# Kernel tuning notes

Measured on AMD Instinct MI355X. Metric: run time of the kernel, lower is better.

## Reference

```python
import jax, jax.numpy as jnp
import numpy as np

B, Q, G, D = 32, 512, 100, 1024
SEED_COST_WEIGHT = 1.0
INF = jnp.float32(1e9)
PAD_COST = jnp.float32(1e3)  # constant cost on padded-GT rows; constant-per-row => does not perturb the valid assignment


def _hungarian(cost):
    """Optimal linear assignment via Jonker-Volgenant shortest augmenting path.
    cost: (n, m) float32 with n <= m. Every row gets a distinct column.
    Returns (m,) int32: 0-based row assigned to each column, -1 if column unassigned.
    Matches scipy.optimize.linear_sum_assignment on the transposed problem."""
    n, m = cost.shape
    cpad = jnp.pad(cost, ((1, 0), (0, 0)))            # 1-based row indexing
    u0 = jnp.zeros(n + 1, cost.dtype)                 # row potentials
    v0 = jnp.zeros(m + 1, cost.dtype)                 # col potentials
    p0 = jnp.zeros(m + 1, jnp.int32)                  # p[j]: 1-based row matched to col j (0 = free)

    def assign_row(i, uvp):
        u, v, p = uvp
        p = p.at[0].set(i)
        state = (u, v, p,
                 jnp.full(m + 1, INF, cost.dtype),    # minv: min reduced cost to reach col j
                 jnp.zeros(m + 1, bool),              # used cols
                 jnp.zeros(m + 1, jnp.int32),         # way: predecessor col on shortest path
                 jnp.int32(0))                        # j0: current col (0 = virtual start)

        def not_free(c):
            _, _, p, _, _, _, j0 = c
            return c[2][j0] != 0

        def step(c):
            u, v, p, minv, used, way, j0 = c
            used = used.at[j0].set(True)
            i0 = p[j0]
            cur = cpad[i0] - u[i0] - v[1:]            # reduced costs of row i0, shape (m,)
            upd = (~used[1:]) & (cur < minv[1:])
            minv = minv.at[1:].set(jnp.where(upd, cur, minv[1:]))
            way = way.at[1:].set(jnp.where(upd, j0, way[1:]))
            masked = jnp.where(used[1:], INF, minv[1:])
            j1 = jnp.argmin(masked).astype(jnp.int32) + 1
            delta = masked[j1 - 1]
            u = u.at[p].add(jnp.where(used, delta, jnp.float32(0.0)))
            v = jnp.where(used, v - delta, v)
            minv = jnp.where(used, minv, minv - delta)
            return (u, v, p, minv, used, way, j1)

        u, v, p, _, _, way, j0 = jax.lax.while_loop(not_free, step, state)

        def backtrack(c):
            j0, p = c
            j1 = way[j0]
            return (j1, p.at[j0].set(p[j1]))

        _, p = jax.lax.while_loop(lambda c: c[0] != 0, backtrack, (j0, p))
        return (u, v, p)

    _, _, p = jax.lax.fori_loop(1, n + 1, assign_row, (u0, v0, p0))
    return p[1:] - 1                                   # (m,) 0-based row per column, -1 if none


def _match(q_sig_flat, gt_sigs_norm, gt_pad_mask, q_seed_logits_flat):
    # Cost built transposed as (B, G, Q): rows = GT slots (n = G <= m = Q).
    # pairwise_similarity(metric='dot'): sim[q, g] = q_sig[q] . gt_sig[g]
    sim = jnp.einsum('bqd,bgd->bgq', q_sig_flat, gt_sigs_norm)   # (B, G, Q)
    cost = 1.0 - sim
    # seed cost is per-query: added to every GT row of that query's column
    cost = cost + SEED_COST_WEIGHT * (1.0 - jax.nn.sigmoid(q_seed_logits_flat))[:, None, :]
    # padded GT rows get a row-constant cost -> assignment over valid rows is unchanged
    cost = jnp.where(gt_pad_mask[:, :, None], cost, PAD_COST)
    row4col = jax.vmap(_hungarian)(jax.lax.stop_gradient(cost))  # (B, Q): GT idx per query
    safe = jnp.maximum(row4col, 0)
    valid = (row4col >= 0) & jnp.take_along_axis(gt_pad_mask, safe, axis=1)
    matched_query_mask = valid                                   # (B, Q) bool
    matched_gt_indices = jnp.where(valid, row4col, -1)           # (B, Q) int32, -1 = unmatched
    return matched_query_mask, matched_gt_indices


def setup_inputs() -> dict:
    key = jax.random.key(0)
    k1, k2, k3, k4 = jax.random.split(key, 4)
    q_sig_flat = jax.random.normal(k1, (B, Q, D), jnp.float32)
    gt = jax.random.normal(k2, (B, G, D), jnp.float32)
    gt_sigs_norm = gt / jnp.linalg.norm(gt, axis=-1, keepdims=True)  # 'norm' suffix -> unit vectors
    gt_pad_mask = jax.random.randint(k3, (B, G), 0, 2).astype(bool)  # True = valid GT
    q_seed_logits_flat = jax.random.normal(k4, (B, Q), jnp.float32)
    return {"q_sig_flat": q_sig_flat, "gt_sigs_norm": gt_sigs_norm,
            "gt_pad_mask": gt_pad_mask, "q_seed_logits_flat": q_seed_logits_flat}


def reference(q_sig_flat, gt_sigs_norm, gt_pad_mask, q_seed_logits_flat):
    return _match(q_sig_flat, gt_sigs_norm, gt_pad_mask, q_seed_logits_flat)
```

## Files before the change

### kernel.cpp

```cpp
#include <hip/hip_runtime.h>
#include <math.h>

#define B_ 32
#define Q_ 512
#define G_ 100
#define D_ 1024
#define INF_ 1.0e9f
#define NVCAP 96

typedef __attribute__((ext_vector_type(8))) short bf16x8;
typedef __attribute__((ext_vector_type(4))) float f32x4;

__device__ __forceinline__ void cvt_hilo(const float* a, bf16x8& hi, bf16x8& lo) {
#pragma unroll
    for (int j = 0; j < 8; ++j) {
        float x = a[j];
        unsigned u  = __float_as_uint(x);
        unsigned hb = (u + 0x7FFFu + ((u >> 16) & 1u)) >> 16;
        float hf = __uint_as_float(hb << 16);
        float r  = x - hf;
        unsigned v  = __float_as_uint(r);
        unsigned lb = (v + 0x7FFFu + ((v >> 16) & 1u)) >> 16;
        hi[j] = (short)hb;
        lo[j] = (short)lb;
    }
}

__global__ __launch_bounds__(512) void cost_kernel(
    const float* __restrict__ qsig, const float* __restrict__ gtm,
    const int* __restrict__ mask, const float* __restrict__ seed,
    float* __restrict__ cost)
{
    __shared__ float pool[27648];
    __shared__ int   vrow_s[128];
    __shared__ int   nv_s;

    const int b   = blockIdx.x;
    const int qt  = blockIdx.y;
    const int tid = threadIdx.x;

    if (tid < 64) {
        int base = 0;
#pragma unroll
        for (int hh = 0; hh < 2; ++hh) {
            int g = hh * 64 + tid;
            int m = (g < G_) ? mask[b * G_ + g] : 0;
            unsigned long long bal = __ballot(m != 0);
            int pre = base + __popcll(bal & ((1ull << tid) - 1ull));
            if (g < G_ && m != 0) vrow_s[pre] = g;
            base += __popcll(bal);
        }
        if (tid == 0) nv_s = (base < NVCAP) ? base : NVCAP;
    }
    __syncthreads();
    const int nv = nv_s;
    if (nv == 0) return;

    const int wid  = tid >> 6;
    const int lane = tid & 63;
    const int h    = wid & 1;
    const int sl   = wid >> 1;
    const int l15  = lane & 15;
    const int l4   = lane >> 4;

    float* qw  = pool + wid * 2304;
    float* gw  = pool + 18432 + wid * 1152;
    float* red = pool;

    const float* qbase = qsig + (size_t)(b * Q_ + qt * 64) * D_;
    const float* gbase = gtm  + (size_t)b * G_ * D_;

#pragma unroll 1
    for (int gtl = 0; gtl * 64 < nv; ++gtl) {
        const int sbase = gtl * 64;

        int grows_st[4];
#pragma unroll
        for (int it = 0; it < 4; ++it) {
            int slv = sbase + h * 32 + it * 8 + (lane >> 3);
            grows_st[it] = vrow_s[(slv < nv) ? slv : (nv - 1)];
        }

        f32x4 acc[2][4];
#pragma unroll
        for (int gi = 0; gi < 2; ++gi)
#pragma unroll
            for (int qj = 0; qj < 4; ++qj) acc[gi][qj] = (f32x4)0.0f;

#pragma unroll 1
        for (int t = 0; t < 8; ++t) {
            const int kt = sl * 256 + t * 32;
#pragma unroll
            for (int it = 0; it < 8; ++it) {
                int row = it * 8 + (lane >> 3);
                float4 v = *(const float4*)(qbase + (size_t)row * D_ + kt + 4 * (lane & 7));
                *(float4*)(qw + row * 36 + 4 * (lane & 7)) = v;
            }
#pragma unroll
            for (int it = 0; it < 4; ++it) {
                int row = it * 8 + (lane >> 3);
                float4 v = *(const float4*)(gbase + (size_t)grows_st[it] * D_ + kt + 4 * (lane & 7));
                *(float4*)(gw + row * 36 + 4 * (lane & 7)) = v;
            }
            bf16x8 bh[4], bl[4];
#pragma unroll
            for (int qj = 0; qj < 4; ++qj) {
                float tmp[8];
                const float* qr = qw + (qj * 16 + l15) * 36 + l4 * 8;
                *(float4*)&tmp[0] = *(const float4*)qr;
                *(float4*)&tmp[4] = *(const float4*)(qr + 4);
                cvt_hilo(tmp, bh[qj], bl[qj]);
            }
#pragma unroll
            for (int gi = 0; gi < 2; ++gi) {
                float tmp[8];
                const float* gr = gw + (gi * 16 + l15) * 36 + l4 * 8;
                *(float4*)&tmp[0] = *(const float4*)gr;
                *(float4*)&tmp[4] = *(const float4*)(gr + 4);
                bf16x8 ah, al;
                cvt_hilo(tmp, ah, al);
#pragma unroll
                for (int qj = 0; qj < 4; ++qj) {
                    acc[gi][qj] = __builtin_amdgcn_mfma_f32_16x16x32_bf16(ah, bh[qj], acc[gi][qj], 0, 0, 0);
                    acc[gi][qj] = __builtin_amdgcn_mfma_f32_16x16x32_bf16(ah, bl[qj], acc[gi][qj], 0, 0, 0);
                    acc[gi][qj] = __builtin_amdgcn_mfma_f32_16x16x32_bf16(al, bh[qj], acc[gi][qj], 0, 0, 0);
                }
            }
        }

        __syncthreads();

        if (sl != 0) {
#pragma unroll
            for (int gi = 0; gi < 2; ++gi)
#pragma unroll
                for (int qj = 0; qj < 4; ++qj)
                    *(f32x4*)(red + wid * 2048 + (gi * 4 + qj) * 256 + lane * 4) = acc[gi][qj];
        }
        __syncthreads();
        if (sl == 0) {
#pragma unroll
            for (int s2 = 1; s2 < 4; ++s2) {
                const int ws = h + 2 * s2;
#pragma unroll
                for (int gi = 0; gi < 2; ++gi)
#pragma unroll
                    for (int qj = 0; qj < 4; ++qj) {
                        f32x4 p = *(const f32x4*)(red + ws * 2048 + (gi * 4 + qj) * 256 + lane * 4);
                        acc[gi][qj] += p;
                    }
            }

            float sc[4];
#pragma unroll
            for (int qj = 0; qj < 4; ++qj) {
                float s   = seed[b * Q_ + qt * 64 + qj * 16 + l15];
                float sig = 1.0f / (1.0f + expf(-s));
                sc[qj] = 1.0f - sig;
            }

            float* tbF = cost + (((size_t)(b * G_ + NVCAP)) << 9);
            int*   tbI = ((int*)tbF) + 1024;

#pragma unroll
            for (int gi = 0; gi < 2; ++gi) {
#pragma unroll
                for (int r = 0; r < 4; ++r) {
                    const int sg = sbase + h * 32 + gi * 16 + l4 * 4 + r;
                    float bv = 3.0e38f; int bq = 0;
#pragma unroll
                    for (int qj = 0; qj < 4; ++qj) {
                        float po = (1.0f - acc[gi][qj][r]) + sc[qj];
                        int   q  = qt * 64 + qj * 16 + l15;
                        if (sg < nv)
                            cost[(((size_t)(b * G_ + sg)) << 9) + q] = po;
                        if (po < bv) { bv = po; bq = q; }
                    }
#pragma unroll
                    for (int off = 1; off <= 8; off <<= 1) {
                        float ov = __shfl_xor(bv, off);
                        int   oq = __shfl_xor(bq, off);
                        if (ov < bv || (ov == bv && oq < bq)) { bv = ov; bq = oq; }
                    }
                    if (l15 == 0 && sg < nv) { tbF[sg * 8 + qt] = bv; tbI[sg * 8 + qt] = bq; }
                }
            }
        }
        __syncthreads();
    }
}

template<int CTRL>
__device__ __forceinline__ float dppmin(float x) {
    int m = __builtin_amdgcn_update_dpp(__float_as_int(x), __float_as_int(x),
                                        CTRL, 0xF, 0xF, false);
    return fminf(x, __int_as_float(m));
}
__device__ __forceinline__ float wave_min64(float x) {
    x = dppmin<0x111>(x);
    x = dppmin<0x112>(x);
    x = dppmin<0x114>(x);
    x = dppmin<0x118>(x);
    x = dppmin<0x142>(x);
    x = dppmin<0x143>(x);
    return __int_as_float(__builtin_amdgcn_readlane(__float_as_int(x), 63));
}
__device__ __forceinline__ int first_col(const float* mval, float vmin) {
    unsigned long long bl[8];
#pragma unroll
    for (int k = 0; k < 8; ++k) bl[k] = __ballot(mval[k] == vmin);
    int j = 511;
    if      (bl[0]) j = (int)__ffsll(bl[0]) - 1;
    else if (bl[1]) j = 64  + (int)__ffsll(bl[1]) - 1;
    else if (bl[2]) j = 128 + (int)__ffsll(bl[2]) - 1;
    else if (bl[3]) j = 192 + (int)__ffsll(bl[3]) - 1;
    else if (bl[4]) j = 256 + (int)__ffsll(bl[4]) - 1;
    else if (bl[5]) j = 320 + (int)__ffsll(bl[5]) - 1;
    else if (bl[6]) j = 384 + (int)__ffsll(bl[6]) - 1;
    else if (bl[7]) j = 448 + (int)__ffsll(bl[7]) - 1;
    return j;
}

__global__ __launch_bounds__(64, 1) void hung_kernel(
    const float* __restrict__ cost, const int* __restrict__ mask,
    int* __restrict__ outp)
{
    __shared__ float u_l[G_ + 4];
    __shared__ int   p_l[Q_ + 4];
    __shared__ int   way_l[Q_];
    __shared__ int   vrow_l[G_ + 4];
    __shared__ int   pend_l[G_ + 4];
    __shared__ int   colw[Q_];
    __shared__ float rmin_s[G_ + 4];
    __shared__ int   rcol_s[G_ + 4];

    const int b    = blockIdx.x;
    const int lane = threadIdx.x;

    for (int r = lane; r <= G_; r += 64) u_l[r] = 0.0f;
    for (int j = lane; j <= Q_; j += 64) p_l[j] = 0;
#pragma unroll
    for (int k = 0; k < 8; ++k) colw[lane + (k << 6)] = 0x7fffffff;

    int base = 0;
#pragma unroll
    for (int h = 0; h < 2; ++h) {
        int g = h * 64 + lane;
        int m = (g < G_) ? mask[b * G_ + g] : 0;
        unsigned long long bal = __ballot(m != 0);
        int pre = base + __popcll(bal & ((1ull << lane) - 1ull));
        if (g < G_ && m != 0) vrow_l[pre] = g;
        base += __popcll(bal);
    }
    const int nv = (base < NVCAP) ? base : NVCAP;
    __syncthreads();

    const float* costb = cost + ((size_t)(b * G_) << 9);
    const float* tbF   = costb + ((size_t)NVCAP << 9);
    const int*   tbI   = ((const int*)tbF) + 1024;

#pragma unroll
    for (int h = 0; h < 2; ++h) {
        int s0 = h * 64 + lane;
        if (s0 < nv) {
            float bv = tbF[s0 * 8];
            int   bq = tbI[s0 * 8];
#pragma unroll
            for (int t = 1; t < 8; ++t) {
                float v = tbF[s0 * 8 + t];
                int   q = tbI[s0 * 8 + t];
                if (v < bv) { bv = v; bq = q; }
            }
            rmin_s[s0] = bv; rcol_s[s0] = bq;
            u_l[s0 + 1] = bv;
        }
    }
    __syncthreads();
#pragma unroll
    for (int h = 0; h < 2; ++h) {
        int s0 = h * 64 + lane;
        if (s0 < nv) atomicMin(&colw[rcol_s[s0]], s0 + 1);
    }
    __syncthreads();
#pragma unroll
    for (int k = 0; k < 8; ++k) {
        int c = lane + (k << 6);
        int w = colw[c];
        p_l[c + 1] = (w == 0x7fffffff) ? 0 : w;
    }
    int npend = 0;
#pragma unroll
    for (int h = 0; h < 2; ++h) {
        int s0 = h * 64 + lane;
        bool pend = (s0 < nv) && (colw[rcol_s[s0]] != s0 + 1);
        unsigned long long bal = __ballot(pend);
        int pre = npend + __popcll(bal & ((1ull << lane) - 1ull));
        if (pend) pend_l[pre] = s0 + 1;
        npend += __popcll(bal);
    }
    __syncthreads();

    float v_r[8], minv_r[8], urow_r[8];
    int   prow_r[8], srow_r[8];
#pragma unroll
    for (int k = 0; k < 8; ++k) {
        int pr = p_l[lane + (k << 6) + 1];
        v_r[k] = 0.0f;
        prow_r[k] = pr;
        urow_r[k] = (pr > 0) ? u_l[pr] : 0.0f;
        srow_r[k] = (pr > 0) ? pr - 1 : 0;
    }

    for (int pi = 0; pi < npend; ++pi) {
        const int i = pend_l[pi];
#pragma unroll
        for (int k = 0; k < 8; ++k) minv_r[k] = INF_;
        unsigned usedm = 0;
        if (lane == 0) p_l[0] = i;
        int   j0  = 0;
        float ui0 = u_l[i];
        int   st  = i - 1;

        while (true) {
            if (j0 > 0) {
                int k0 = (j0 - 1) >> 6;
                if (lane == ((j0 - 1) & 63)) usedm |= (1u << k0);
            }
            const float* src = costb + ((size_t)st << 9);
            float cstv[8];
#pragma unroll
            for (int k = 0; k < 8; ++k) cstv[k] = src[lane + (k << 6)];
            float mval[8];
#pragma unroll
            for (int k = 0; k < 8; ++k) {
                if (usedm & (1u << k)) {
                    mval[k] = INF_;
                } else {
                    float cur = (cstv[k] - ui0) - v_r[k];
                    if (cur < minv_r[k]) { minv_r[k] = cur; way_l[lane + (k << 6)] = j0; }
                    mval[k] = minv_r[k];
                }
            }
            float x = fminf(fminf(fminf(mval[0], mval[1]), fminf(mval[2], mval[3])),
                            fminf(fminf(mval[4], mval[5]), fminf(mval[6], mval[7])));
            const float vmin  = wave_min64(x);
            const int   j1col = first_col(mval, vmin);
            const float delta = vmin;
            const int   j1    = j1col + 1;
            const int   k1    = j1col >> 6;
            const int   ol    = j1col & 63;

            int pn_c = prow_r[0], st_c = srow_r[0]; float un_c = urow_r[0];
#pragma unroll
            for (int k = 1; k < 8; ++k) {
                bool sel = (k1 == k);
                pn_c = sel ? prow_r[k] : pn_c;
                un_c = sel ? urow_r[k] : un_c;
                st_c = sel ? srow_r[k] : st_c;
            }
            const int   pn  = __shfl(pn_c, ol);
            const float uin = __shfl(un_c, ol);
            const int   stn = __shfl(st_c, ol);

#pragma unroll
            for (int k = 0; k < 8; ++k) {
                if (usedm & (1u << k)) { v_r[k] -= delta; urow_r[k] += delta; }
                else                   { minv_r[k] -= delta; }
            }
#pragma unroll
            for (int k = 0; k < 8; ++k)
                if (usedm & (1u << k)) u_l[prow_r[k]] += delta;
            if (lane == 0) u_l[i] += delta;

            j0 = j1; ui0 = uin; st = stn;
            if (pn == 0) break;
        }
        const int fincol = j0 - 1;
        __syncthreads();
        if (lane == 0) {
            int j = j0;
            while (j != 0) { int wj = way_l[j - 1]; p_l[j] = p_l[wj]; j = wj; }
        }
        __syncthreads();
#pragma unroll
        for (int k = 0; k < 8; ++k) {
            int c = lane + (k << 6);
            if ((usedm & (1u << k)) || (c == fincol)) {
                int pr = p_l[c + 1];
                prow_r[k] = pr;
                urow_r[k] = u_l[pr];
                srow_r[k] = (pr > 0) ? pr - 1 : 0;
            }
        }
    }

#pragma unroll
    for (int k = 0; k < 8; ++k) {
        int c = lane + (k << 6);
        int r = p_l[c + 1];
        outp[b * Q_ + c]           = (r > 0) ? 1 : 0;
        outp[B_ * Q_ + b * Q_ + c] = (r > 0) ? vrow_l[r - 1] : -1;
    }
}

extern "C" void kernel_launch(void* const* d_in, const int* in_sizes, int n_in,
                              void* d_out, int out_size, void* d_ws, size_t ws_size,
                              hipStream_t stream) {
    (void)in_sizes; (void)n_in; (void)out_size; (void)ws_size;
    const float* qsig = (const float*)d_in[0];
    const float* gtm  = (const float*)d_in[1];
    const int*   mask = (const int*)d_in[2];
    const float* seed = (const float*)d_in[3];
    float* cost = (float*)d_ws;
    int*   outp = (int*)d_out;

    cost_kernel<<<dim3(32, 8), 512, 0, stream>>>(qsig, gtm, mask, seed, cost);
    hung_kernel<<<dim3(32), 64, 0, stream>>>(cost, mask, outp);
}
```

Baseline: 49.79 us.

## Halve query tile per block and register-prefetch next K slice

The cost kernel now handles 32 queries per block instead of 64, doubling the grid to 32x16 blocks and shrinking shared memory so more blocks can run at once. The global loads for the next K slice are prefetched into registers while the current slice is converted and multiplied, hiding load latency. The per-row min/argmin table moves to a fixed workspace offset with 16 entries per row, and the assignment kernel reads all 16. In exchange the GT rows are reloaded by twice as many blocks, and more registers are held for the prefetch.

```diff
diff --git a/kernel.cpp b/kernel.cpp
--- a/kernel.cpp
+++ b/kernel.cpp
@@ -7,6 +7,8 @@
 #define D_ 1024
 #define INF_ 1.0e9f
 #define NVCAP 96
+#define TBF_OFF 1638400
+#define TBI_OFF 1687552
 
 typedef __attribute__((ext_vector_type(8))) short bf16x8;
 typedef __attribute__((ext_vector_type(4))) float f32x4;
@@ -31,7 +33,7 @@
     const int* __restrict__ mask, const float* __restrict__ seed,
     float* __restrict__ cost)
 {
-    __shared__ float pool[27648];
+    __shared__ float pool[18432];
     __shared__ int   vrow_s[128];
     __shared__ int   nv_s;
 
@@ -62,12 +64,14 @@
     const int sl   = wid >> 1;
     const int l15  = lane & 15;
     const int l4   = lane >> 4;
-
-    float* qw  = pool + wid * 2304;
-    float* gw  = pool + 18432 + wid * 1152;
+    const int srow = lane >> 3;
+    const int sk4  = lane & 7;
+
+    float* qw  = pool + wid * 1152;
+    float* gw  = pool + 9216 + wid * 1152;
     float* red = pool;
 
-    const float* qbase = qsig + (size_t)(b * Q_ + qt * 64) * D_;
+    const float* qbase = qsig + (size_t)(b * Q_ + qt * 32) * D_;
     const float* gbase = gtm  + (size_t)b * G_ * D_;
 
 #pragma unroll 1
@@ -77,34 +81,44 @@
         int grows_st[4];
 #pragma unroll
         for (int it = 0; it < 4; ++it) {
-            int slv = sbase + h * 32 + it * 8 + (lane >> 3);
+            int slv = sbase + h * 32 + it * 8 + srow;
             grows_st[it] = vrow_s[(slv < nv) ? slv : (nv - 1)];
         }
 
-        f32x4 acc[2][4];
+        f32x4 acc[2][2];
 #pragma unroll
         for (int gi = 0; gi < 2; ++gi)
 #pragma unroll
-            for (int qj = 0; qj < 4; ++qj) acc[gi][qj] = (f32x4)0.0f;
+            for (int qj = 0; qj < 2; ++qj) acc[gi][qj] = (f32x4)0.0f;
+
+        float4 qp[4], gp[4];
+#pragma unroll
+        for (int it = 0; it < 4; ++it) {
+            int row = it * 8 + srow;
+            qp[it] = *(const float4*)(qbase + (size_t)row * D_ + sl * 256 + 4 * sk4);
+            gp[it] = *(const float4*)(gbase + (size_t)grows_st[it] * D_ + sl * 256 + 4 * sk4);
+        }
 
 #pragma unroll 1
         for (int t = 0; t < 8; ++t) {
-            const int kt = sl * 256 + t * 32;
-#pragma unroll
-            for (int it = 0; it < 8; ++it) {
-                int row = it * 8 + (lane >> 3);
-                float4 v = *(const float4*)(qbase + (size_t)row * D_ + kt + 4 * (lane & 7));
-                *(float4*)(qw + row * 36 + 4 * (lane & 7)) = v;
-            }
 #pragma unroll
             for (int it = 0; it < 4; ++it) {
-                int row = it * 8 + (lane >> 3);
-                float4 v = *(const float4*)(gbase + (size_t)grows_st[it] * D_ + kt + 4 * (lane & 7));
-                *(float4*)(gw + row * 36 + 4 * (lane & 7)) = v;
-            }
-            bf16x8 bh[4], bl[4];
-#pragma unroll
-            for (int qj = 0; qj < 4; ++qj) {
+                int row = it * 8 + srow;
+                *(float4*)(qw + row * 36 + 4 * sk4) = qp[it];
+                *(float4*)(gw + row * 36 + 4 * sk4) = gp[it];
+            }
+            if (t < 7) {
+                int kt2 = sl * 256 + (t + 1) * 32;
+#pragma unroll
+                for (int it = 0; it < 4; ++it) {
+                    int row = it * 8 + srow;
+                    qp[it] = *(const float4*)(qbase + (size_t)row * D_ + kt2 + 4 * sk4);
+                    gp[it] = *(const float4*)(gbase + (size_t)grows_st[it] * D_ + kt2 + 4 * sk4);
+                }
+            }
+            bf16x8 bh[2], bl[2];
+#pragma unroll
+            for (int qj = 0; qj < 2; ++qj) {
                 float tmp[8];
                 const float* qr = qw + (qj * 16 + l15) * 36 + l4 * 8;
                 *(float4*)&tmp[0] = *(const float4*)qr;
@@ -120,7 +134,7 @@
                 bf16x8 ah, al;
                 cvt_hilo(tmp, ah, al);
 #pragma unroll
-                for (int qj = 0; qj < 4; ++qj) {
+                for (int qj = 0; qj < 2; ++qj) {
                     acc[gi][qj] = __builtin_amdgcn_mfma_f32_16x16x32_bf16(ah, bh[qj], acc[gi][qj], 0, 0, 0);
                     acc[gi][qj] = __builtin_amdgcn_mfma_f32_16x16x32_bf16(ah, bl[qj], acc[gi][qj], 0, 0, 0);
                     acc[gi][qj] = __builtin_amdgcn_mfma_f32_16x16x32_bf16(al, bh[qj], acc[gi][qj], 0, 0, 0);
@@ -134,8 +148,8 @@
 #pragma unroll
             for (int gi = 0; gi < 2; ++gi)
 #pragma unroll
-                for (int qj = 0; qj < 4; ++qj)
-                    *(f32x4*)(red + wid * 2048 + (gi * 4 + qj) * 256 + lane * 4) = acc[gi][qj];
+                for (int qj = 0; qj < 2; ++qj)
+                    *(f32x4*)(red + wid * 1024 + (gi * 2 + qj) * 256 + lane * 4) = acc[gi][qj];
         }
         __syncthreads();
         if (sl == 0) {
@@ -145,22 +159,22 @@
 #pragma unroll
                 for (int gi = 0; gi < 2; ++gi)
 #pragma unroll
-                    for (int qj = 0; qj < 4; ++qj) {
-                        f32x4 p = *(const f32x4*)(red + ws * 2048 + (gi * 4 + qj) * 256 + lane * 4);
+                    for (int qj = 0; qj < 2; ++qj) {
+                        f32x4 p = *(const f32x4*)(red + ws * 1024 + (gi * 2 + qj) * 256 + lane * 4);
                         acc[gi][qj] += p;
                     }
             }
 
-            float sc[4];
-#pragma unroll
-            for (int qj = 0; qj < 4; ++qj) {
-                float s   = seed[b * Q_ + qt * 64 + qj * 16 + l15];
+            float sc[2];
+#pragma unroll
+            for (int qj = 0; qj < 2; ++qj) {
+                float s   = seed[b * Q_ + qt * 32 + qj * 16 + l15];
                 float sig = 1.0f / (1.0f + expf(-s));
                 sc[qj] = 1.0f - sig;
             }
 
-            float* tbF = cost + (((size_t)(b * G_ + NVCAP)) << 9);
-            int*   tbI = ((int*)tbF) + 1024;
+            float* tbF = cost + TBF_OFF + b * 1536;
+            int*   tbI = ((int*)(cost + TBI_OFF)) + b * 1536;
 
 #pragma unroll
             for (int gi = 0; gi < 2; ++gi) {
@@ -169,9 +183,9 @@
                     const int sg = sbase + h * 32 + gi * 16 + l4 * 4 + r;
                     float bv = 3.0e38f; int bq = 0;
 #pragma unroll
-                    for (int qj = 0; qj < 4; ++qj) {
+                    for (int qj = 0; qj < 2; ++qj) {
                         float po = (1.0f - acc[gi][qj][r]) + sc[qj];
-                        int   q  = qt * 64 + qj * 16 + l15;
+                        int   q  = qt * 32 + qj * 16 + l15;
                         if (sg < nv)
                             cost[(((size_t)(b * G_ + sg)) << 9) + q] = po;
                         if (po < bv) { bv = po; bq = q; }
@@ -182,7 +196,7 @@
                         int   oq = __shfl_xor(bq, off);
                         if (ov < bv || (ov == bv && oq < bq)) { bv = ov; bq = oq; }
                     }
-                    if (l15 == 0 && sg < nv) { tbF[sg * 8 + qt] = bv; tbI[sg * 8 + qt] = bq; }
+                    if (l15 == 0 && sg < nv) { tbF[sg * 16 + qt] = bv; tbI[sg * 16 + qt] = bq; }
                 }
             }
         }
@@ -256,19 +270,19 @@
     __syncthreads();
 
     const float* costb = cost + ((size_t)(b * G_) << 9);
-    const float* tbF   = costb + ((size_t)NVCAP << 9);
-    const int*   tbI   = ((const int*)tbF) + 1024;
+    const float* tbF   = cost + TBF_OFF + b * 1536;
+    const int*   tbI   = ((const int*)(cost + TBI_OFF)) + b * 1536;
 
 #pragma unroll
     for (int h = 0; h < 2; ++h) {
         int s0 = h * 64 + lane;
         if (s0 < nv) {
-            float bv = tbF[s0 * 8];
-            int   bq = tbI[s0 * 8];
-#pragma unroll
-            for (int t = 1; t < 8; ++t) {
-                float v = tbF[s0 * 8 + t];
-                int   q = tbI[s0 * 8 + t];
+            float bv = tbF[s0 * 16];
+            int   bq = tbI[s0 * 16];
+#pragma unroll
+            for (int t = 1; t < 16; ++t) {
+                float v = tbF[s0 * 16 + t];
+                int   q = tbI[s0 * 16 + t];
                 if (v < bv) { bv = v; bq = q; }
             }
             rmin_s[s0] = bv; rcol_s[s0] = bq;
@@ -414,6 +428,6 @@
     float* cost = (float*)d_ws;
     int*   outp = (int*)d_out;
 
-    cost_kernel<<<dim3(32, 8), 512, 0, stream>>>(qsig, gtm, mask, seed, cost);
+    cost_kernel<<<dim3(32, 16), 512, 0, stream>>>(qsig, gtm, mask, seed, cost);
     hung_kernel<<<dim3(32), 64, 0, stream>>>(cost, mask, outp);
 }
```

Measured after the change: 100.7 us. 2.02x slower.
